# Kernel optimization log

Measured on AMD Instinct MI355X. Metric: run time of the kernel, lower is better.

Reference implementation:

```python
import jax, jax.numpy as jnp
import numpy as np

BSZ = 2048   # number of graphs
DIM = 256    # node feature dim


def setup_inputs() -> dict:
    rng = np.random.default_rng(0)
    sizes = rng.integers(64, 193, size=BSZ)          # variable graph sizes
    total = int(sizes.sum())                          # ~262K nodes
    key = jax.random.key(0)
    graph_embedding = jax.random.normal(key, (total, DIM), dtype=jnp.float32)
    graph_len = jnp.asarray(sizes, dtype=jnp.int32)
    return {"graph_embedding": graph_embedding, "graph_len": graph_len}


def reference(graph_embedding, graph_len):
    # Original pads each graph to max_size with zeros, then means over dim=1.
    # Equivalent: per-graph segment sum divided by max(graph_len).
    bsz = graph_len.shape[0]
    n = graph_embedding.shape[0]
    seg_ids = jnp.repeat(jnp.arange(bsz), graph_len, total_repeat_length=n)
    sums = jax.ops.segment_sum(graph_embedding, seg_ids, num_segments=bsz)  # [bsz, dim]
    max_size = jnp.max(graph_len).astype(graph_embedding.dtype)
    return sums / max_size
```

## Files before the change

### kernel.cpp

```cpp
#include <hip/hip_runtime.h>

#define BSZ 2048
#define DIM 256

__global__ __launch_bounds__(256) void graph_mean_kernel(
    const float* __restrict__ emb,
    const int*   __restrict__ len,
    float*       __restrict__ out)
{
    const int b   = blockIdx.x;
    const int tid = threadIdx.x;

    __shared__ int s_off[256];
    __shared__ int s_max[256];

    int po = 0, pm = 0;
    for (int i = tid; i < BSZ; i += 256) {
        int l = len[i];
        if (i < b) po += l;
        pm = max(pm, l);
    }
    s_off[tid] = po;
    s_max[tid] = pm;
    __syncthreads();
    #pragma unroll
    for (int s = 128; s > 0; s >>= 1) {
        if (tid < s) {
            s_off[tid] += s_off[tid + s];
            s_max[tid]  = max(s_max[tid], s_max[tid + s]);
        }
        __syncthreads();
    }
    const int   start   = s_off[0];
    const int   mylen   = len[b];
    const float inv_max = 1.0f / (float)s_max[0];
    __syncthreads();

    const int cg = tid & 63;
    const int rg = tid >> 6;

    float4 acc = make_float4(0.f, 0.f, 0.f, 0.f);
    const float* base = emb + (size_t)start * DIM + (size_t)cg * 4;
    for (int r = rg; r < mylen; r += 4) {
        const float4 v = *reinterpret_cast<const float4*>(base + (size_t)r * DIM);
        acc.x += v.x; acc.y += v.y; acc.z += v.z; acc.w += v.w;
    }

    __shared__ float4 s_part[4][64];
    s_part[rg][cg] = acc;
    __syncthreads();

    if (rg == 0) {
        const float4 a0 = s_part[0][cg];
        const float4 a1 = s_part[1][cg];
        const float4 a2 = s_part[2][cg];
        const float4 a3 = s_part[3][cg];
        float4 r;
        r.x = (a0.x + a1.x + a2.x + a3.x) * inv_max;
        r.y = (a0.y + a1.y + a2.y + a3.y) * inv_max;
        r.z = (a0.z + a1.z + a2.z + a3.z) * inv_max;
        r.w = (a0.w + a1.w + a2.w + a3.w) * inv_max;
        *reinterpret_cast<float4*>(out + (size_t)b * DIM + (size_t)cg * 4) = r;
    }
}

extern "C" void kernel_launch(void* const* d_in, const int* in_sizes, int n_in,
                              void* d_out, int out_size, void* d_ws, size_t ws_size,
                              hipStream_t stream) {
    const float* emb = (const float*)d_in[0];
    const int*   len = (const int*)d_in[1];
    float*       out = (float*)d_out;

    graph_mean_kernel<<<BSZ, 256, 0, stream>>>(emb, len, out);
}
```

Before: 50.03 us.

## Split into prefix-scan kernel and row-balanced segment sum with atomics

Replaces the per-graph block design, where every block redundantly scans all lengths, with a single-block scan kernel that writes offsets and the max length to workspace. A second kernel splits the rows evenly across blocks and finds each block's starting graph by binary search. Segments that cross chunk boundaries are combined with float atomics into an output zeroed by a memset. This balances work across blocks regardless of graph size, at the cost of two extra launches, atomics on boundary segments, and a dependency on the scan.

Result: slower. 59.17 us (+18.3%).

```diff
diff --git a/kernel.cpp b/kernel.cpp
--- a/kernel.cpp
+++ b/kernel.cpp
@@ -2,65 +2,103 @@
 
 #define BSZ 2048
 #define DIM 256
+#define NB  2048
 
-__global__ __launch_bounds__(256) void graph_mean_kernel(
-    const float* __restrict__ emb,
-    const int*   __restrict__ len,
-    float*       __restrict__ out)
+
+__global__ __launch_bounds__(256) void scan_kernel(const int* __restrict__ len,
+                                                   int* __restrict__ ws_i)
 {
-    const int b   = blockIdx.x;
-    const int tid = threadIdx.x;
+    const int t = threadIdx.x;
+    int loc[8];
+    int run = 0, mymax = 0;
+    #pragma unroll
+    for (int j = 0; j < 8; ++j) {
+        const int l = len[t * 8 + j];
+        run += l;
+        loc[j] = run;
+        mymax = max(mymax, l);
+    }
 
-    __shared__ int s_off[256];
-    __shared__ int s_max[256];
+    __shared__ int s[256];
+    __shared__ int smax[256];
+    s[t] = run;
+    smax[t] = mymax;
+    __syncthreads();
+    for (int d = 1; d < 256; d <<= 1) {
+        const int v = (t >= d) ? s[t - d] : 0;
+        const int m = (t >= d) ? smax[t - d] : 0;
+        __syncthreads();
+        s[t] += v;
+        smax[t] = max(smax[t], m);
+        __syncthreads();
+    }
+    const int base = s[t] - run;
+    if (t == 0) ws_i[0] = 0;
+    #pragma unroll
+    for (int j = 0; j < 8; ++j) ws_i[t * 8 + j + 1] = base + loc[j];
+    if (t == 255) ws_i[BSZ + 1] = smax[255];
+}
 
-    int po = 0, pm = 0;
-    for (int i = tid; i < BSZ; i += 256) {
-        int l = len[i];
-        if (i < b) po += l;
-        pm = max(pm, l);
+__global__ __launch_bounds__(256) void sum_kernel(const float* __restrict__ emb,
+                                                  const int* __restrict__ ws_i,
+                                                  float* __restrict__ out,
+                                                  int N, int chunk)
+{
+    const int r0 = blockIdx.x * chunk;
+    if (r0 >= N) return;
+    const int r1 = min(r0 + chunk, N);
+
+    const float inv_max = 1.0f / (float)ws_i[BSZ + 1];
+
+    int lo = 0, hi = BSZ - 1;
+    while (lo < hi) {
+        const int mid = (lo + hi + 1) >> 1;
+        if (ws_i[mid] <= r0) lo = mid; else hi = mid - 1;
     }
-    s_off[tid] = po;
-    s_max[tid] = pm;
-    __syncthreads();
-    #pragma unroll
-    for (int s = 128; s > 0; s >>= 1) {
-        if (tid < s) {
-            s_off[tid] += s_off[tid + s];
-            s_max[tid]  = max(s_max[tid], s_max[tid + s]);
+    int g = lo;
+
+    const int cg = threadIdx.x & 63;
+    const int rg = threadIdx.x >> 6;
+    __shared__ float4 s_part[4][64];
+
+    int row = r0;
+    while (row < r1) {
+        const int seg_start = ws_i[g];
+        const int seg_end_g = ws_i[g + 1];
+        const int seg_end   = min(seg_end_g, r1);
+
+        float4 acc = make_float4(0.f, 0.f, 0.f, 0.f);
+        const float* base = emb + (size_t)cg * 4;
+        for (int r = row + rg; r < seg_end; r += 4) {
+            const float4 v = *reinterpret_cast<const float4*>(base + (size_t)r * DIM);
+            acc.x += v.x; acc.y += v.y; acc.z += v.z; acc.w += v.w;
+        }
+
+        s_part[rg][cg] = acc;
+        __syncthreads();
+        if (rg == 0) {
+            const float4 a0 = s_part[0][cg];
+            const float4 a1 = s_part[1][cg];
+            const float4 a2 = s_part[2][cg];
+            const float4 a3 = s_part[3][cg];
+            float4 r;
+            r.x = (a0.x + a1.x + a2.x + a3.x) * inv_max;
+            r.y = (a0.y + a1.y + a2.y + a3.y) * inv_max;
+            r.z = (a0.z + a1.z + a2.z + a3.z) * inv_max;
+            r.w = (a0.w + a1.w + a2.w + a3.w) * inv_max;
+            float* o = out + (size_t)g * DIM + (size_t)cg * 4;
+            if (seg_start >= r0 && seg_end_g <= r1) {
+                *reinterpret_cast<float4*>(o) = r;
+            } else {
+                atomicAdd(o + 0, r.x);
+                atomicAdd(o + 1, r.y);
+                atomicAdd(o + 2, r.z);
+                atomicAdd(o + 3, r.w);
+            }
         }
         __syncthreads();
-    }
-    const int   start   = s_off[0];
-    const int   mylen   = len[b];
-    const float inv_max = 1.0f / (float)s_max[0];
-    __syncthreads();
-
-    const int cg = tid & 63;
-    const int rg = tid >> 6;
-
-    float4 acc = make_float4(0.f, 0.f, 0.f, 0.f);
-    const float* base = emb + (size_t)start * DIM + (size_t)cg * 4;
-    for (int r = rg; r < mylen; r += 4) {
-        const float4 v = *reinterpret_cast<const float4*>(base + (size_t)r * DIM);
-        acc.x += v.x; acc.y += v.y; acc.z += v.z; acc.w += v.w;
-    }
-
-    __shared__ float4 s_part[4][64];
-    s_part[rg][cg] = acc;
-    __syncthreads();
-
-    if (rg == 0) {
-        const float4 a0 = s_part[0][cg];
-        const float4 a1 = s_part[1][cg];
-        const float4 a2 = s_part[2][cg];
-        const float4 a3 = s_part[3][cg];
-        float4 r;
-        r.x = (a0.x + a1.x + a2.x + a3.x) * inv_max;
-        r.y = (a0.y + a1.y + a2.y + a3.y) * inv_max;
-        r.z = (a0.z + a1.z + a2.z + a3.z) * inv_max;
-        r.w = (a0.w + a1.w + a2.w + a3.w) * inv_max;
-        *reinterpret_cast<float4*>(out + (size_t)b * DIM + (size_t)cg * 4) = r;
+        row = seg_end;
+        ++g;
     }
 }
 
@@ -70,6 +108,12 @@
     const float* emb = (const float*)d_in[0];
     const int*   len = (const int*)d_in[1];
     float*       out = (float*)d_out;
+    int*         wsi = (int*)d_ws;
 
-    graph_mean_kernel<<<BSZ, 256, 0, stream>>>(emb, len, out);
+    const int N = in_sizes[0] / DIM;
+    const int chunk = (N + NB - 1) / NB;
+
+    hipMemsetAsync(out, 0, (size_t)out_size * sizeof(float), stream);
+    scan_kernel<<<1, 256, 0, stream>>>(len, wsi);
+    sum_kernel<<<NB, 256, 0, stream>>>(emb, wsi, out, N, chunk);
 }
```
